# Kernel optimization log

Measured on AMD Instinct MI355X. Metric: run time of the kernel, lower is better.

## Reference

```python
import jax, jax.numpy as jnp
import numpy as np

L, B, C, S = 4, 256, 512, 64   # layers, batch, channels, spatial (8x8 pooled map)
N = 50000                      # training-bank size per layer
K = 20                         # neighbors for LID


def setup_inputs() -> dict:
    key = jax.random.key(0)
    k1, k2 = jax.random.split(key)
    feats = jax.random.normal(k1, (L, B, C, S), dtype=jnp.float32)
    bank = jax.random.normal(k2, (L, N, C), dtype=jnp.float32)
    return {"feats": feats, "bank": bank, "k": K}


def reference(feats, bank, k):
    # per-layer spatial mean pool: f.view(B, C, -1).mean(dim=2)
    q = feats.mean(axis=-1)                                   # [L, B, C]
    # pairwise Euclidean distances query-vs-bank per layer
    q2 = jnp.sum(q * q, axis=-1)                              # [L, B]
    b2 = jnp.sum(bank * bank, axis=-1)                        # [L, N]
    cross = jnp.einsum('lbc,lnc->lbn', q, bank)               # [L, B, N]
    d2 = q2[:, :, None] + b2[:, None, :] - 2.0 * cross
    dist = jnp.sqrt(jnp.maximum(d2, 0.0))                     # [L, B, N]
    # k+1 smallest distances, ascending (sklearn kneighbors), drop nearest
    neg_top, _ = jax.lax.top_k(-dist, k + 1)                  # [L, B, k+1]
    dk = -neg_top[..., 1:]                                    # [L, B, k] ascending
    r_k = dk[..., -1:]                                        # k-th NN distance
    logs = jnp.log(dk / r_k)                                  # [L, B, k]
    lids = -(k / jnp.sum(logs, axis=-1))                      # [L, B]
    return jnp.transpose(lids, (1, 0))                        # [B, L]
```

## Files before the change

### kernel.cpp

```cpp
#include <hip/hip_runtime.h>
#include <hip/hip_bf16.h>

#define L_ 4
#define B_ 256
#define C_ 512
#define N_ 50000
#define K_ 20
#define NLIST 21
#define NCH 128
#define BIGF 3.0e38f
#define BN 64
#define KS 32
#define NKS 16

#define QS0_O 0u
#define QS1_O 16384u
#define BS0_O 32768u
#define BS1_O 36864u
#define B2P_O 40960u
#define B2V_O 43008u
#define SMEM_BYTES 45056

typedef __attribute__((ext_vector_type(8))) short short8;
typedef __attribute__((ext_vector_type(4))) float f32x4;

__device__ __forceinline__ unsigned pk2(float lo, float hi) {
    __hip_bfloat162 h = __float22bfloat162_rn(make_float2(lo, hi));
    return *reinterpret_cast<unsigned*>(&h);
}
__device__ __forceinline__ float sq4(float4 v) {
    return v.x*v.x + v.y*v.y + v.z*v.z + v.w*v.w;
}

#define LGKM_BAR() do { asm volatile("s_waitcnt lgkmcnt(0)" ::: "memory"); \
                        __builtin_amdgcn_s_barrier(); } while (0)

__global__ void qmean_kernel(const float* __restrict__ feats,
                             unsigned short* __restrict__ qbf)
{
    int gtid = blockIdx.x * 256 + threadIdx.x;
    int wid  = gtid >> 6;
    int lane = threadIdx.x & 63;
    const float4* src = reinterpret_cast<const float4*>(feats) + (size_t)wid * 64 + lane;
    float4 v = *src;
    float s = v.x + v.y + v.z + v.w;
    s += __shfl_xor(s, 1); s += __shfl_xor(s, 2);
    s += __shfl_xor(s, 4); s += __shfl_xor(s, 8);
    if ((lane & 15) == 0) {
        __hip_bfloat16 h = __float2bfloat16(s * (1.0f / 64.0f));
        qbf[wid * 4 + (lane >> 4)] = *reinterpret_cast<unsigned short*>(&h);
    }
}

__global__ __launch_bounds__(512, 4)
void dist_topk_kernel(const float* __restrict__ bank,
                      const unsigned short* __restrict__ qbf,
                      float* __restrict__ lists)
{
    __shared__ __align__(16) unsigned char smem[SMEM_BYTES];
    float* sd  = reinterpret_cast<float*>(smem);
    float* b2p = reinterpret_cast<float*>(smem + B2P_O);
    float* b2v = reinterpret_cast<float*>(smem + B2V_O);
    float* mg  = reinterpret_cast<float*>(smem);

    const int tid = threadIdx.x;
    const int l   = blockIdx.x >> 7;
    const int nc  = blockIdx.x & 127;

    const unsigned short* qg = qbf + (size_t)l * B_ * C_;
    const float* bb = bank + (size_t)l * N_ * C_;
    const int n0 = (nc * 3125) >> 3;
    const int n1 = ((nc + 1) * 3125) >> 3;

    const int lane = tid & 63;
    const int wv   = tid >> 6;
    const int c_lo = lane & 15;
    const int r_hi = lane >> 4;

    int q_src[2]; unsigned q_dst[2];
#pragma unroll
    for (int j = 0; j < 2; ++j) {
        const int i = tid + 512*j, row = i >> 2, slot = i & 3;
        q_src[j] = row * C_ + ((slot ^ ((row >> 1) & 3)) << 3);
        q_dst[j] = (unsigned)i << 4;
    }
    const int brow   = tid >> 3;
    const int b_srck = ((((tid >> 1) & 3) ^ ((brow >> 1) & 3)) << 3) + ((tid & 1) << 2);
    const unsigned b_dst = (unsigned)tid << 3;

    unsigned offA[2], offB[4];
#pragma unroll
    for (int m = 0; m < 2; ++m) {
        const int row = wv*32 + m*16 + c_lo;
        offA[m] = (unsigned)(row*64 + ((r_hi ^ ((row >> 1) & 3)) << 4));
    }
#pragma unroll
    for (int n = 0; n < 4; ++n) {
        const int row = n*16 + c_lo;
        offB[n] = (unsigned)(row*64 + ((r_hi ^ ((row >> 1) & 3)) << 4));
    }

#define LOADQ(dst, kb) do { \
        dst[0] = *reinterpret_cast<const short8*>(qg + q_src[0] + (kb)); \
        dst[1] = *reinterpret_cast<const short8*>(qg + q_src[1] + (kb)); } while (0)
#define LOADB(dst, ntt, kb) do { \
        dst = make_float4(0.f, 0.f, 0.f, 0.f); \
        const int gr_ = (ntt) + brow; \
        if (gr_ < n1) dst = *reinterpret_cast<const float4*>(bb + (size_t)gr_*C_ + (kb) + b_srck); \
    } while (0)
#define WRITEQ(off, src) do { \
        *reinterpret_cast<short8*>(smem + (off) + q_dst[0]) = src[0]; \
        *reinterpret_cast<short8*>(smem + (off) + q_dst[1]) = src[1]; } while (0)
#define WRITEB(off, v) do { \
        b2a += sq4(v); \
        uint2 pk_; pk_.x = pk2(v.x, v.y); pk_.y = pk2(v.z, v.w); \
        *reinterpret_cast<uint2*>(smem + (off) + b_dst) = pk_; } while (0)
#define DO_MFMA(qoff, boff) do { \
        const short8 a0_ = *reinterpret_cast<const short8*>(smem + (qoff) + offA[0]); \
        const short8 a1_ = *reinterpret_cast<const short8*>(smem + (qoff) + offA[1]); \
        _Pragma("unroll") \
        for (int n_ = 0; n_ < 4; ++n_) { \
            const short8 bn_ = *reinterpret_cast<const short8*>(smem + (boff) + offB[n_]); \
            acc[0][n_] = __builtin_amdgcn_mfma_f32_16x16x32_bf16(a0_, bn_, acc[0][n_], 0, 0, 0); \
            acc[1][n_] = __builtin_amdgcn_mfma_f32_16x16x32_bf16(a1_, bn_, acc[1][n_], 0, 0, 0); \
        } } while (0)

    float list[NLIST];
#pragma unroll
    for (int i = 0; i < NLIST; ++i) list[i] = BIGF;

    short8 qva[2], qvb[2];
    float4 bva, bvb;
    LOADQ(qva, 0);
    LOADB(bva, n0, 0);

#pragma unroll 1
    for (int nt = n0; nt < n1; nt += BN) {
        f32x4 acc[2][4];
#pragma unroll
        for (int m = 0; m < 2; ++m)
#pragma unroll
            for (int n = 0; n < 4; ++n) acc[m][n] = (f32x4){0.f, 0.f, 0.f, 0.f};
        float b2a = 0.f;

        LOADQ(qvb, KS);
        LOADB(bvb, nt, KS);
        WRITEQ(QS0_O, qva);
        WRITEB(BS0_O, bva);
        LGKM_BAR();

#pragma unroll 1
        for (int ks = 0; ks < NKS; ks += 2) {
            WRITEQ(QS1_O, qvb);
            WRITEB(BS1_O, bvb);
            if (ks + 2 < NKS) {
                LOADQ(qva, (ks + 2) * KS);
                LOADB(bva, nt, (ks + 2) * KS);
            } else if (nt + BN < n1) {
                LOADQ(qva, 0);
                LOADB(bva, nt + BN, 0);
            }
            DO_MFMA(QS0_O, BS0_O);
            LGKM_BAR();
            if (ks + 3 < NKS) {
                LOADQ(qvb, (ks + 3) * KS);
                LOADB(bvb, nt, (ks + 3) * KS);
            }
            if (ks + 2 < NKS) {
                WRITEQ(QS0_O, qva);
                WRITEB(BS0_O, bva);
            }
            DO_MFMA(QS1_O, BS1_O);
            LGKM_BAR();
        }

        b2p[tid] = b2a;
        LGKM_BAR();
        if (tid < 64) {
            const float* p = b2p + tid*8;
            b2v[tid] = ((p[0]+p[1]) + (p[2]+p[3])) + ((p[4]+p[5]) + (p[6]+p[7]));
        }
        LGKM_BAR();

#pragma unroll
        for (int ph = 0; ph < 2; ++ph) {
#pragma unroll
            for (int m = 0; m < 2; ++m)
#pragma unroll
                for (int nn = 0; nn < 2; ++nn) {
                    const int n    = 2*ph + nn;
                    const int col  = 16*n + c_lo;
                    const int lcol = 16*nn + c_lo;
                    const float bv = b2v[col];
                    const bool ok  = (nt + col) < n1;
#pragma unroll
                    for (int rg = 0; rg < 4; ++rg) {
                        const int row = wv*32 + m*16 + r_hi*4 + rg;
                        const float v = fmaf(-2.0f, acc[m][n][rg], bv);
                        sd[row*34 + lcol] = ok ? v : BIGF;
                    }
                }
            LGKM_BAR();
            {
                const float* srow = sd + (tid >> 1)*34 + ((tid & 1) << 4);
#pragma unroll
                for (int bt = 0; bt < 4; ++bt) {
                    const float2 u = *reinterpret_cast<const float2*>(srow + (bt << 2));
                    const float2 w = *reinterpret_cast<const float2*>(srow + (bt << 2) + 2);
                    const float m4 = fminf(fminf(u.x, u.y), fminf(w.x, w.y));
                    if (m4 < list[NLIST-1]) {
                        float cand[4] = {u.x, u.y, w.x, w.y};
#pragma unroll
                        for (int c4 = 0; c4 < 4; ++c4) {
                            float v = cand[c4];
                            if (v < list[NLIST-1]) {
#pragma unroll
                                for (int i = 0; i < NLIST; ++i) {
                                    const float lo = fminf(list[i], v);
                                    const float hi = fmaxf(list[i], v);
                                    list[i] = lo; v = hi;
                                }
                            }
                        }
                    }
                }
            }
            LGKM_BAR();
        }
    }

#pragma unroll
    for (int i = 0; i < NLIST; ++i) mg[tid*22 + i] = list[i];
    LGKM_BAR();
    if ((tid & 1) == 0) {
        const int row = tid >> 1;
        float* outp = lists + ((size_t)(l*B_ + row)*NCH + nc)*NLIST;
        const float* g0 = mg + tid*22;
        const float* g1 = mg + (tid + 1)*22;
        int p0 = 0, p1 = 0;
#pragma unroll 1
        for (int i = 0; i < NLIST; ++i) {
            const float h0 = (p0 < NLIST) ? g0[p0] : BIGF;
            const float h1 = (p1 < NLIST) ? g1[p1] : BIGF;
            if (h0 <= h1) { outp[i] = h0; ++p0; }
            else          { outp[i] = h1; ++p1; }
        }
    }
#undef LOADQ
#undef LOADB
#undef WRITEQ
#undef WRITEB
#undef DO_MFMA
}

__global__ void lid_kernel(const float* __restrict__ lists,
                           const unsigned short* __restrict__ qbf,
                           float* __restrict__ out)
{
    __shared__ float pops[4][NLIST];
    const int lane = threadIdx.x & 63;
    const int w    = threadIdx.x >> 6;
    const int gw   = blockIdx.x * 4 + w;
    const int l    = gw & 3;
    const int b    = gw >> 2;

    const unsigned short* qr = qbf + ((size_t)l*B_ + b)*C_;
    short8 qv = *reinterpret_cast<const short8*>(qr + lane*8);
    float q2 = 0.f;
#pragma unroll
    for (int i = 0; i < 8; ++i) {
        unsigned u = ((unsigned)(unsigned short)qv[i]) << 16;
        float f = __uint_as_float(u);
        q2 += f*f;
    }
    q2 += __shfl_xor(q2,1); q2 += __shfl_xor(q2,2); q2 += __shfl_xor(q2,4);
    q2 += __shfl_xor(q2,8); q2 += __shfl_xor(q2,16); q2 += __shfl_xor(q2,32);

    const float* base = lists + (size_t)(l*B_ + b) * NCH * NLIST;
    int p0 = 0, p1 = 0;
#pragma unroll 1
    for (int i = 0; i < NLIST; ++i) {
        const float h0 = (p0 < NLIST) ? base[(size_t)lane*NLIST + p0] : BIGF;
        const float h1 = (p1 < NLIST) ? base[(size_t)(lane+64)*NLIST + p1] : BIGF;
        const float h  = fminf(h0, h1);
        float m = h;
        m = fminf(m, __shfl_xor(m,1));  m = fminf(m, __shfl_xor(m,2));
        m = fminf(m, __shfl_xor(m,4));  m = fminf(m, __shfl_xor(m,8));
        m = fminf(m, __shfl_xor(m,16)); m = fminf(m, __shfl_xor(m,32));
        const unsigned long long ball = __ballot(h == m);
        if (lane == __ffsll(ball) - 1) {
            if (h0 == m) ++p0;
            else         ++p1;
        }
        if (lane == 0) pops[w][i] = fmaxf(q2 + m, 0.f);
    }
    __syncthreads();

    const float r2 = pops[w][NLIST-1];
    float t = 0.f;
    if (lane >= 1 && lane < NLIST) t = 0.5f * logf(pops[w][lane] / r2);
    t += __shfl_xor(t,1); t += __shfl_xor(t,2); t += __shfl_xor(t,4);
    t += __shfl_xor(t,8); t += __shfl_xor(t,16); t += __shfl_xor(t,32);

    if (lane == 0) out[(size_t)b * L_ + l] = -(float)K_ / t;
}

extern "C" void kernel_launch(void* const* d_in, const int* in_sizes, int n_in,
                              void* d_out, int out_size, void* d_ws, size_t ws_size,
                              hipStream_t stream)
{
    (void)in_sizes; (void)n_in; (void)out_size; (void)ws_size;
    const float* feats = (const float*)d_in[0];
    const float* bank  = (const float*)d_in[1];
    unsigned short* qbf = (unsigned short*)d_ws;
    float* lists = (float*)((char*)d_ws + (size_t)L_*B_*C_*2);

    qmean_kernel<<<32768, 256, 0, stream>>>(feats, qbf);
    dist_topk_kernel<<<L_*NCH, 512, 0, stream>>>(bank, qbf, lists);
    lid_kernel<<<256, 256, 0, stream>>>(lists, qbf, (float*)d_out);
}
```

Baseline: 261.5 us.

## Load query fragments directly from pre-swizzled global layout and deepen bank prefetch

The qmean kernel now writes bf16 query means in an MFMA-fragment-ordered layout, so the distance kernel reads A operands straight from global/L2 into registers instead of staging them through LDS. The bank tile pipeline is restructured into a fully unrolled 16-step loop with a 4-deep register prefetch ring and clamped addresses instead of bounds branches. Row norms are reduced with shuffles rather than an LDS pass. This cuts LDS traffic and barriers per K-step and raises memory-level parallelism, at the cost of more registers and per-step global query loads. The loop trip count is fixed at 7 tiles.

```diff
diff --git a/kernel.cpp b/kernel.cpp
--- a/kernel.cpp
+++ b/kernel.cpp
@@ -12,13 +12,12 @@
 #define BN 64
 #define KS 32
 #define NKS 16
-
-#define QS0_O 0u
-#define QS1_O 16384u
-#define BS0_O 32768u
-#define BS1_O 36864u
-#define B2P_O 40960u
-#define B2V_O 43008u
+#define NT_ 7
+
+#define BS0_O 0u
+#define BS1_O 4096u
+#define B2V_O 8192u
+#define SD_O  8448u
 #define SMEM_BYTES 45056
 
 typedef __attribute__((ext_vector_type(8))) short short8;
@@ -47,8 +46,17 @@
     s += __shfl_xor(s, 1); s += __shfl_xor(s, 2);
     s += __shfl_xor(s, 4); s += __shfl_xor(s, 8);
     if ((lane & 15) == 0) {
+        const int flat = wid * 4 + (lane >> 4);
+        const int c    = flat & (C_ - 1);
+        const int rowg = flat >> 9;
+        const int l    = rowg >> 8;
+        const int b    = rowg & (B_ - 1);
+        const int kb = c >> 5, rh = (c >> 3) & 3, e = c & 7;
+        const int band = b >> 5, m = (b >> 4) & 1, cl = b & 15;
+        const size_t idx =
+            ((size_t)(((l*16 + kb)*8 + band)*2 + m)*4 + rh)*128 + cl*8 + e;
         __hip_bfloat16 h = __float2bfloat16(s * (1.0f / 64.0f));
-        qbf[wid * 4 + (lane >> 4)] = *reinterpret_cast<unsigned short*>(&h);
+        qbf[idx] = *reinterpret_cast<unsigned short*>(&h);
     }
 }
 
@@ -58,127 +66,108 @@
                       float* __restrict__ lists)
 {
     __shared__ __align__(16) unsigned char smem[SMEM_BYTES];
-    float* sd  = reinterpret_cast<float*>(smem);
-    float* b2p = reinterpret_cast<float*>(smem + B2P_O);
     float* b2v = reinterpret_cast<float*>(smem + B2V_O);
+    float* sd  = reinterpret_cast<float*>(smem + SD_O);
     float* mg  = reinterpret_cast<float*>(smem);
 
     const int tid = threadIdx.x;
     const int l   = blockIdx.x >> 7;
     const int nc  = blockIdx.x & 127;
 
-    const unsigned short* qg = qbf + (size_t)l * B_ * C_;
     const float* bb = bank + (size_t)l * N_ * C_;
-    const int n0 = (nc * 3125) >> 3;
-    const int n1 = ((nc + 1) * 3125) >> 3;
+    const int n0   = (nc * 3125) >> 3;
+    const int n1   = ((nc + 1) * 3125) >> 3;
+    const int n1m1 = n1 - 1;
 
     const int lane = tid & 63;
     const int wv   = tid >> 6;
     const int c_lo = lane & 15;
     const int r_hi = lane >> 4;
 
-    int q_src[2]; unsigned q_dst[2];
-#pragma unroll
-    for (int j = 0; j < 2; ++j) {
-        const int i = tid + 512*j, row = i >> 2, slot = i & 3;
-        q_src[j] = row * C_ + ((slot ^ ((row >> 1) & 3)) << 3);
-        q_dst[j] = (unsigned)i << 4;
-    }
+    const unsigned short* qf0 = qbf + (size_t)l * 131072 + wv * 1024 + lane * 8;
+    const unsigned short* qf1 = qf0 + 512;
+
     const int brow   = tid >> 3;
     const int b_srck = ((((tid >> 1) & 3) ^ ((brow >> 1) & 3)) << 3) + ((tid & 1) << 2);
     const unsigned b_dst = (unsigned)tid << 3;
 
-    unsigned offA[2], offB[4];
-#pragma unroll
-    for (int m = 0; m < 2; ++m) {
-        const int row = wv*32 + m*16 + c_lo;
-        offA[m] = (unsigned)(row*64 + ((r_hi ^ ((row >> 1) & 3)) << 4));
-    }
+    unsigned offB[4];
 #pragma unroll
     for (int n = 0; n < 4; ++n) {
         const int row = n*16 + c_lo;
         offB[n] = (unsigned)(row*64 + ((r_hi ^ ((row >> 1) & 3)) << 4));
     }
 
-#define LOADQ(dst, kb) do { \
-        dst[0] = *reinterpret_cast<const short8*>(qg + q_src[0] + (kb)); \
-        dst[1] = *reinterpret_cast<const short8*>(qg + q_src[1] + (kb)); } while (0)
-#define LOADB(dst, ntt, kb) do { \
-        dst = make_float4(0.f, 0.f, 0.f, 0.f); \
-        const int gr_ = (ntt) + brow; \
-        if (gr_ < n1) dst = *reinterpret_cast<const float4*>(bb + (size_t)gr_*C_ + (kb) + b_srck); \
-    } while (0)
-#define WRITEQ(off, src) do { \
-        *reinterpret_cast<short8*>(smem + (off) + q_dst[0]) = src[0]; \
-        *reinterpret_cast<short8*>(smem + (off) + q_dst[1]) = src[1]; } while (0)
-#define WRITEB(off, v) do { \
-        b2a += sq4(v); \
-        uint2 pk_; pk_.x = pk2(v.x, v.y); pk_.y = pk2(v.z, v.w); \
-        *reinterpret_cast<uint2*>(smem + (off) + b_dst) = pk_; } while (0)
-#define DO_MFMA(qoff, boff) do { \
-        const short8 a0_ = *reinterpret_cast<const short8*>(smem + (qoff) + offA[0]); \
-        const short8 a1_ = *reinterpret_cast<const short8*>(smem + (qoff) + offA[1]); \
-        _Pragma("unroll") \
-        for (int n_ = 0; n_ < 4; ++n_) { \
-            const short8 bn_ = *reinterpret_cast<const short8*>(smem + (boff) + offB[n_]); \
-            acc[0][n_] = __builtin_amdgcn_mfma_f32_16x16x32_bf16(a0_, bn_, acc[0][n_], 0, 0, 0); \
-            acc[1][n_] = __builtin_amdgcn_mfma_f32_16x16x32_bf16(a1_, bn_, acc[1][n_], 0, 0, 0); \
-        } } while (0)
-
     float list[NLIST];
 #pragma unroll
     for (int i = 0; i < NLIST; ++i) list[i] = BIGF;
 
-    short8 qva[2], qvb[2];
-    float4 bva, bvb;
-    LOADQ(qva, 0);
-    LOADB(bva, n0, 0);
+    float4 rr[4];
+    short8 qa, qb_;
+    float  b2a = 0.f, b2_keep = 0.f;
+
+    {
+        const float* ba0 = bb + (size_t)min(n0 + brow, n1m1) * C_ + b_srck;
+#pragma unroll
+        for (int s4 = 0; s4 < 4; ++s4)
+            rr[s4] = *reinterpret_cast<const float4*>(
+                reinterpret_cast<const char*>(ba0) + s4 * (KS * 4));
+        const float4 v = rr[0];
+        b2a = sq4(v);
+        uint2 pk_; pk_.x = pk2(v.x, v.y); pk_.y = pk2(v.z, v.w);
+        *reinterpret_cast<uint2*>(smem + BS0_O + b_dst) = pk_;
+        qa  = *reinterpret_cast<const short8*>(qf0);
+        qb_ = *reinterpret_cast<const short8*>(qf1);
+        LGKM_BAR();
+    }
 
 #pragma unroll 1
-    for (int nt = n0; nt < n1; nt += BN) {
+    for (int t = 0; t < NT_; ++t) {
+        const int nt = n0 + t * BN;
+        const float* baddrA = bb + (size_t)min(nt + brow,      n1m1) * C_ + b_srck;
+        const float* baddrB = bb + (size_t)min(nt + BN + brow, n1m1) * C_ + b_srck;
+
         f32x4 acc[2][4];
 #pragma unroll
         for (int m = 0; m < 2; ++m)
 #pragma unroll
             for (int n = 0; n < 4; ++n) acc[m][n] = (f32x4){0.f, 0.f, 0.f, 0.f};
-        float b2a = 0.f;
-
-        LOADQ(qvb, KS);
-        LOADB(bvb, nt, KS);
-        WRITEQ(QS0_O, qva);
-        WRITEB(BS0_O, bva);
-        LGKM_BAR();
-
-#pragma unroll 1
-        for (int ks = 0; ks < NKS; ks += 2) {
-            WRITEQ(QS1_O, qvb);
-            WRITEB(BS1_O, bvb);
-            if (ks + 2 < NKS) {
-                LOADQ(qva, (ks + 2) * KS);
-                LOADB(bva, nt, (ks + 2) * KS);
-            } else if (nt + BN < n1) {
-                LOADQ(qva, 0);
-                LOADB(bva, nt + BN, 0);
-            }
-            DO_MFMA(QS0_O, BS0_O);
+
+#pragma unroll
+        for (int s = 0; s < NKS; ++s) {
+            {
+                const float4 v = rr[(s + 1) & 3];
+                const float s2 = sq4(v);
+                if (s == NKS - 1) { b2_keep = b2a; b2a = s2; } else b2a += s2;
+                uint2 pk_; pk_.x = pk2(v.x, v.y); pk_.y = pk2(v.z, v.w);
+                *reinterpret_cast<uint2*>(smem + ((s + 1) & 1 ? BS1_O : BS0_O) + b_dst) = pk_;
+            }
+            {
+                const float* ba = (s >= NKS - 4) ? baddrB : baddrA;
+                rr[s & 3] = *reinterpret_cast<const float4*>(
+                    reinterpret_cast<const char*>(ba) + ((s + 4) & 15) * (KS * 4));
+            }
+            {
+                const unsigned bso = (s & 1) ? BS1_O : BS0_O;
+#pragma unroll
+                for (int n = 0; n < 4; ++n) {
+                    const short8 bn = *reinterpret_cast<const short8*>(smem + bso + offB[n]);
+                    acc[0][n] = __builtin_amdgcn_mfma_f32_16x16x32_bf16(qa,  bn, acc[0][n], 0, 0, 0);
+                    acc[1][n] = __builtin_amdgcn_mfma_f32_16x16x32_bf16(qb_, bn, acc[1][n], 0, 0, 0);
+                }
+            }
+            {
+                const int kb2 = ((s + 1) & 15) * 8192;
+                qa  = *reinterpret_cast<const short8*>(qf0 + kb2);
+                qb_ = *reinterpret_cast<const short8*>(qf1 + kb2);
+            }
             LGKM_BAR();
-            if (ks + 3 < NKS) {
-                LOADQ(qvb, (ks + 3) * KS);
-                LOADB(bvb, nt, (ks + 3) * KS);
-            }
-            if (ks + 2 < NKS) {
-                WRITEQ(QS0_O, qva);
-                WRITEB(BS0_O, bva);
-            }
-            DO_MFMA(QS1_O, BS1_O);
-            LGKM_BAR();
-        }
-
-        b2p[tid] = b2a;
-        LGKM_BAR();
-        if (tid < 64) {
-            const float* p = b2p + tid*8;
-            b2v[tid] = ((p[0]+p[1]) + (p[2]+p[3])) + ((p[4]+p[5]) + (p[6]+p[7]));
+        }
+
+        {
+            float v = b2_keep;
+            v += __shfl_xor(v, 1); v += __shfl_xor(v, 2); v += __shfl_xor(v, 4);
+            if ((tid & 7) == 0) b2v[brow] = v;
         }
         LGKM_BAR();
 
@@ -246,11 +235,6 @@
             else          { outp[i] = h1; ++p1; }
         }
     }
-#undef LOADQ
-#undef LOADB
-#undef WRITEQ
-#undef WRITEB
-#undef DO_MFMA
 }
 
 __global__ void lid_kernel(const float* __restrict__ lists,
@@ -264,8 +248,10 @@
     const int l    = gw & 3;
     const int b    = gw >> 2;
 
-    const unsigned short* qr = qbf + ((size_t)l*B_ + b)*C_;
-    short8 qv = *reinterpret_cast<const short8*>(qr + lane*8);
+    const size_t qidx =
+        ((size_t)(((l*16 + (lane >> 2))*8 + (b >> 5))*2 + ((b >> 4) & 1))*4 + (lane & 3))*128
+        + (size_t)(b & 15)*8;
+    short8 qv = *reinterpret_cast<const short8*>(qbf + qidx);
     float q2 = 0.f;
 #pragma unroll
     for (int i = 0; i < 8; ++i) {
```

Result: slower. 268.7 us (+2.7%).
